# Optimization experiments

Measured on AMD Instinct MI355X. Metric: run time of the kernel, lower is better.

## Reference

```python
import jax, jax.numpy as jnp
import numpy as np

N, T = 1024, 32
D_FEAT, GATE_START, GATE_END = 158, 158, 221
D_MODEL = 256
T_NHEAD, S_NHEAD = 4, 2
BETA = 5.0
LN_EPS = 1e-5


def _ln(x, g, b):
    mu = jnp.mean(x, axis=-1, keepdims=True)
    var = jnp.mean(jnp.square(x - mu), axis=-1, keepdims=True)
    return (x - mu) * jax.lax.rsqrt(var + LN_EPS) * g + b


def _pos_enc(t, d):
    pos = jnp.arange(t, dtype=jnp.float32)[:, None]
    div = jnp.exp(jnp.arange(0, d, 2, dtype=jnp.float32) * (-np.log(10000.0) / d))
    pe = jnp.zeros((t, d), dtype=jnp.float32)
    pe = pe.at[:, 0::2].set(jnp.sin(pos * div))
    pe = pe.at[:, 1::2].set(jnp.cos(pos * div))
    return pe


def _mha(xn, qw, kw, vw, nhead, temperature):
    # xn: [B, S, D] (already layer-normed); attention over axis S
    B, S, D = xn.shape
    dh = D // nhead
    q = (xn @ qw.T).reshape(B, S, nhead, dh)
    k = (xn @ kw.T).reshape(B, S, nhead, dh)
    v = (xn @ vw.T).reshape(B, S, nhead, dh)
    scores = jnp.einsum('bshd,bthd->bhst', q, k) / temperature
    a = jax.nn.softmax(scores, axis=-1)
    return jnp.einsum('bhst,bthd->bshd', a, v).reshape(B, S, D)


def _block(x, qw, kw, vw, n1g, n1b, n2g, n2b, f1w, f1b, f2w, f2b, nhead, temperature):
    xn = _ln(x, n1g, n1b)
    xt = xn + _mha(xn, qw, kw, vw, nhead, temperature)
    xt = _ln(xt, n2g, n2b)
    ffn = jnp.maximum(xt @ f1w.T + f1b, 0.0) @ f2w.T + f2b
    return xt + ffn


def _forward(x, gate_w, gate_b, proj_w, proj_b,
             tq, tk, tv, tn1g, tn1b, tn2g, tn2b, tf1w, tf1b, tf2w, tf2b,
             sq, sk, sv, sn1g, sn1b, sn2g, sn2b, sf1w, sf1b, sf2w, sf2b,
             temp_w, out_w, out_b):
    src = x[:, :, :GATE_START]                     # [N, T, d_feat]
    gate_in = x[:, -1, GATE_START:GATE_END]        # [N, d_gate]
    gate = D_FEAT * jax.nn.softmax((gate_in @ gate_w.T + gate_b) / BETA, axis=-1)
    src = src * gate[:, None, :]
    z = src @ proj_w.T + proj_b                    # [N, T, d_model]
    z = z + _pos_enc(z.shape[1], D_MODEL)
    # TAttention: attend over time, unscaled scores (temperature=1)
    z = _block(z, tq, tk, tv, tn1g, tn1b, tn2g, tn2b, tf1w, tf1b, tf2w, tf2b,
               T_NHEAD, 1.0)
    # SAttention: attend over stocks, temperature = sqrt(d_model/nhead)
    zs = _block(z.swapaxes(0, 1), sq, sk, sv, sn1g, sn1b, sn2g, sn2b,
                sf1w, sf1b, sf2w, sf2b, S_NHEAD, float(np.sqrt(D_MODEL / S_NHEAD)))
    z = zs.swapaxes(0, 1)                          # [N, T, d_model]
    # TemporalAttention pooling
    h = z @ temp_w.T
    lam = jax.nn.softmax(jnp.einsum('ntd,nd->nt', h, h[:, -1, :]), axis=1)
    pooled = jnp.einsum('nt,ntd->nd', lam, z)
    return (pooled @ out_w.T + out_b).squeeze(-1)  # [N]


def setup_inputs() -> dict:
    key = jax.random.key(0)
    ks = iter(jax.random.split(key, 32))
    s = 0.02
    d, f, g = D_MODEL, D_FEAT, GATE_END - GATE_START
    inp = {
        'x': jax.random.normal(next(ks), (N, T, GATE_END), dtype=jnp.float32),
        'gate_w': jax.random.normal(next(ks), (f, g)) * s,
        'gate_b': jnp.zeros((f,)),
        'proj_w': jax.random.normal(next(ks), (d, f)) * s,
        'proj_b': jnp.zeros((d,)),
        'tq': jax.random.normal(next(ks), (d, d)) * s,
        'tk': jax.random.normal(next(ks), (d, d)) * s,
        'tv': jax.random.normal(next(ks), (d, d)) * s,
        'tn1g': jnp.ones((d,)), 'tn1b': jnp.zeros((d,)),
        'tn2g': jnp.ones((d,)), 'tn2b': jnp.zeros((d,)),
        'tf1w': jax.random.normal(next(ks), (d, d)) * s, 'tf1b': jnp.zeros((d,)),
        'tf2w': jax.random.normal(next(ks), (d, d)) * s, 'tf2b': jnp.zeros((d,)),
        'sq': jax.random.normal(next(ks), (d, d)) * s,
        'sk': jax.random.normal(next(ks), (d, d)) * s,
        'sv': jax.random.normal(next(ks), (d, d)) * s,
        'sn1g': jnp.ones((d,)), 'sn1b': jnp.zeros((d,)),
        'sn2g': jnp.ones((d,)), 'sn2b': jnp.zeros((d,)),
        'sf1w': jax.random.normal(next(ks), (d, d)) * s, 'sf1b': jnp.zeros((d,)),
        'sf2w': jax.random.normal(next(ks), (d, d)) * s, 'sf2b': jnp.zeros((d,)),
        'temp_w': jax.random.normal(next(ks), (d, d)) * s,
        'out_w': jax.random.normal(next(ks), (1, d)) * s,
        'out_b': jnp.zeros((1,)),
    }
    return {k: v.astype(jnp.float32) for k, v in inp.items()}


def reference(x, gate_w, gate_b, proj_w, proj_b,
              tq, tk, tv, tn1g, tn1b, tn2g, tn2b, tf1w, tf1b, tf2w, tf2b,
              sq, sk, sv, sn1g, sn1b, sn2g, sn2b, sf1w, sf1b, sf2w, sf2b,
              temp_w, out_w, out_b):
    return _forward(x, gate_w, gate_b, proj_w, proj_b,
                    tq, tk, tv, tn1g, tn1b, tn2g, tn2b, tf1w, tf1b, tf2w, tf2b,
                    sq, sk, sv, sn1g, sn1b, sn2g, sn2b, sf1w, sf1b, sf2w, sf2b,
                    temp_w, out_w, out_b)
```

## Files before the change

### kernel.cpp

```cpp
#include <hip/hip_runtime.h>
#include <math.h>

#define NB   1024
#define TSEQ 32
#define DM   256
#define DF   158
#define GDIM 63
#define XROW 221

typedef unsigned short u16;
typedef __attribute__((ext_vector_type(8))) __bf16 bf16x8;
typedef __attribute__((ext_vector_type(4))) float f32x4;
#define MFMA16(a,b,c) __builtin_amdgcn_mfma_f32_16x16x32_bf16(a,b,c,0,0,0)

#define MODE_QKVT 1
#define MODE_QKVS 2

__device__ __forceinline__ u16 f2bf(float f){
  union { float f; unsigned int u; } c; c.f = f;
  unsigned int u = c.u;
  u += 0x7fffu + ((u >> 16) & 1u);
  return (u16)(u >> 16);
}

__device__ __forceinline__ u16 f2bf_t(float f){
  union { float f; unsigned int u; } c; c.f = f;
  return (u16)(c.u >> 16);
}

__device__ __forceinline__ void gl2lds16(const u16* g, u16* lds_wave_base, int lane){
#if __has_builtin(__builtin_amdgcn_global_load_lds)
  __builtin_amdgcn_global_load_lds(
      (const __attribute__((address_space(1))) unsigned int*)g,
      (__attribute__((address_space(3))) unsigned int*)lds_wave_base,
      16, 0, 0);
#else
  *reinterpret_cast<uint4*>(lds_wave_base + lane * 8) =
      *reinterpret_cast<const uint4*>(g);
#endif
}

#define WB_TOT 770048

__global__ __launch_bounds__(256) void kConvAll(
    const float* __restrict__ tq, const float* __restrict__ tk, const float* __restrict__ tv,
    const float* __restrict__ sq, const float* __restrict__ sk, const float* __restrict__ sv,
    const float* __restrict__ tf1, const float* __restrict__ tf2,
    const float* __restrict__ sf1, const float* __restrict__ sf2,
    const float* __restrict__ tw, const float* __restrict__ pw,
    u16* __restrict__ WB)
{
  int i = blockIdx.x * 256 + threadIdx.x;
  if (i >= WB_TOT) return;
  if (i < 720896){
    int j = i >> 16, o = i & 65535;
    const float* s;
    switch (j){
      case 0: s = tq; break;  case 1: s = tk; break;  case 2: s = tv; break;
      case 3: s = sq; break;  case 4: s = sk; break;  case 5: s = sv; break;
      case 6: s = tf1; break; case 7: s = tf2; break;
      case 8: s = sf1; break; case 9: s = sf2; break;
      default: s = tw; break;
    }
    WB[i] = f2bf(s[o]);
  } else {
    int k = i - 720896;
    int row = k / 192, col = k - row * 192;
    WB[i] = (col < DF) ? f2bf(pw[row * DF + col]) : (u16)0;
  }
}


__global__ __launch_bounds__(256) void kGateSrc(
    const float* __restrict__ x,
    const float* __restrict__ gate_w, const float* __restrict__ gate_b,
    u16* __restrict__ SRC)
{
  __shared__ float s_gate[DF];
  __shared__ float s_gi[GDIM];
  const int tid = threadIdx.x;
  const int n = blockIdx.x;

  if (tid < GDIM) s_gi[tid] = x[(n * TSEQ + (TSEQ - 1)) * XROW + DF + tid];
  __syncthreads();
  float logit = 0.f;
  if (tid < DF){
    logit = gate_b[tid];
    const float* __restrict__ wr = gate_w + tid * GDIM;
    for (int g = 0; g < GDIM; ++g) logit += s_gi[g] * wr[g];
    logit *= 0.2f;
    s_gate[tid] = logit;
  }
  __syncthreads();
  {
    float mx = -1e30f;
    for (int f = 0; f < DF; ++f) mx = fmaxf(mx, s_gate[f]);
    float sm = 0.f;
    for (int f = 0; f < DF; ++f) sm += __expf(s_gate[f] - mx);
    __syncthreads();
    if (tid < DF) s_gate[tid] = (float)DF * __expf(logit - mx) / sm;
  }
  __syncthreads();

  for (int e = tid; e < TSEQ * 192; e += 256){
    int t = e / 192, f = e - t * 192;
    float v = 0.f;
    if (f < DF) v = x[(n * TSEQ + t) * XROW + f] * s_gate[f];
    SRC[(size_t)(n * TSEQ + t) * 192 + f] = f2bf(v);
  }
}


__global__ __launch_bounds__(512) void kProjLN(
    const u16* __restrict__ SRC, const u16* __restrict__ Bw,
    const float* __restrict__ bias,
    const float* __restrict__ lg, const float* __restrict__ lb,
    u16* __restrict__ Xb, float* __restrict__ Xf)
{
  __shared__ alignas(16) u16 sA[128 * 64];
  __shared__ alignas(16) u16 sB[256 * 64];
  __shared__ float s_sum[4 * 128], s_sq[4 * 128];
  __shared__ float s_lg[256], s_lb[256], s_bias[256];

  const int tid = threadIdx.x;
  const int wv = tid >> 6, lane = tid & 63;
  const int wr = wv >> 2, wc = wv & 3;
  const int quad = lane >> 4, lc = lane & 15;
  const int m0 = blockIdx.x * 128;

  if (tid < 256){ s_lg[tid] = lg[tid]; s_lb[tid] = lb[tid]; s_bias[tid] = bias[tid]; }

  f32x4 acc[4][4];
  #pragma unroll
  for (int i = 0; i < 4; ++i)
    #pragma unroll
    for (int j = 0; j < 4; ++j) acc[i][j] = (f32x4){0.f,0.f,0.f,0.f};

  for (int kt = 0; kt < 192; kt += 64){
    __syncthreads();
    #pragma unroll
    for (int i = 0; i < 2; ++i){
      int c = tid + i * 512;
      int row = c >> 3, blk = c & 7;
      *reinterpret_cast<uint4*>(&sA[row * 64 + ((blk ^ (row & 7)) * 8)]) =
        *reinterpret_cast<const uint4*>(SRC + (size_t)(m0 + row) * 192 + kt + blk * 8);
    }
    #pragma unroll
    for (int i = 0; i < 4; ++i){
      int c = tid + i * 512;
      int row = c >> 3, blk = c & 7;
      *reinterpret_cast<uint4*>(&sB[row * 64 + ((blk ^ (row & 7)) * 8)]) =
        *reinterpret_cast<const uint4*>(Bw + (size_t)row * 192 + kt + blk * 8);
    }
    __syncthreads();
    #pragma unroll
    for (int kc = 0; kc < 2; ++kc){
      const int sw = ((kc * 4 + quad) ^ (lc & 7)) * 8;
      bf16x8 a[4], b[4];
      #pragma unroll
      for (int i = 0; i < 4; ++i){
        a[i] = *reinterpret_cast<const bf16x8*>(&sA[(wr * 64 + i * 16 + lc) * 64 + sw]);
        b[i] = *reinterpret_cast<const bf16x8*>(&sB[(wc * 64 + i * 16 + lc) * 64 + sw]);
      }
      #pragma unroll
      for (int i = 0; i < 4; ++i)
        #pragma unroll
        for (int j = 0; j < 4; ++j)
          acc[i][j] = MFMA16(a[i], b[j], acc[i][j]);
    }
  }

  const int rb = wr * 64 + quad * 4;
  #pragma unroll
  for (int i = 0; i < 4; ++i)
    #pragma unroll
    for (int r = 0; r < 4; ++r){
      int rowl = rb + i * 16 + r;
      float ft = (float)((m0 + rowl) & 31);
      float ps = 0.f, pq = 0.f;
      #pragma unroll
      for (int j = 0; j < 4; ++j){
        int col = wc * 64 + j * 16 + lc;
        float div = __expf((float)(col & ~1) * -0.035977892f);
        float ang = ft * div;
        float pe = (col & 1) ? __cosf(ang) : __sinf(ang);
        float v = acc[i][j][r] + s_bias[col] + pe;
        acc[i][j][r] = v;
        ps += v; pq += v * v;
      }
      #pragma unroll
      for (int msk = 1; msk < 16; msk <<= 1){
        ps += __shfl_xor(ps, msk);
        pq += __shfl_xor(pq, msk);
      }
      if (lc == 0){ s_sum[wc * 128 + rowl] = ps; s_sq[wc * 128 + rowl] = pq; }
    }
  __syncthreads();

  #pragma unroll
  for (int i = 0; i < 4; ++i)
    #pragma unroll
    for (int r = 0; r < 4; ++r){
      int rowl = rb + i * 16 + r;
      float sum = s_sum[rowl] + s_sum[128 + rowl] + s_sum[256 + rowl] + s_sum[384 + rowl];
      float sq  = s_sq[rowl]  + s_sq[128 + rowl]  + s_sq[256 + rowl]  + s_sq[384 + rowl];
      float mu = sum * (1.f / 256.f);
      float rs = rsqrtf(sq * (1.f / 256.f) - mu * mu + 1e-5f);
      size_t base = (size_t)(m0 + rowl) * 256;
      #pragma unroll
      for (int j = 0; j < 4; ++j){
        int col = wc * 64 + j * 16 + lc;
        float xn = (acc[i][j][r] - mu) * rs * s_lg[col] + s_lb[col];
        Xf[base + col] = xn;
        Xb[base + col] = f2bf(xn);
      }
    }
}


__global__ __launch_bounds__(256) void gemm_bf16(
    const u16* __restrict__ A, const u16* __restrict__ B,
    const int K, const int mode,
    u16* __restrict__ ob0, u16* __restrict__ ob1, u16* __restrict__ ob2)
{
  __shared__ alignas(16) u16 sA[128 * 64];
  __shared__ alignas(16) u16 sB[128 * 64];
  const int tid = threadIdx.x;
  const int wv = tid >> 6, lane = tid & 63;
  const int wr = wv >> 1, wc = wv & 1;
  const int quad = lane >> 4, lc = lane & 15;
  const int n0 = blockIdx.y * 128;
  const bool tmaj = (mode == MODE_QKVS);
  const int tt = tmaj ? (blockIdx.x & 31) : 0;
  const int nb = tmaj ? (blockIdx.x >> 5) : 0;
  const int m0 = tmaj ? 0 : blockIdx.x * 128;

  f32x4 acc[4][4];
  #pragma unroll
  for (int i = 0; i < 4; ++i)
    #pragma unroll
    for (int j = 0; j < 4; ++j) acc[i][j] = (f32x4){0.f,0.f,0.f,0.f};

  for (int kt = 0; kt < K; kt += 64){
    __syncthreads();
    #pragma unroll
    for (int j = 0; j < 4; ++j){
      int c = wv * 64 + lane + j * 256;
      int row = c >> 3, blk = c & 7;
      int arow = tmaj ? ((nb * 128 + row) * 32 + tt) : (m0 + row);
      gl2lds16(A + (size_t)arow * K + kt + ((blk ^ (row & 7)) * 8),
               &sA[(wv * 64 + j * 256) * 8], lane);
      gl2lds16(B + (size_t)(n0 + row) * K + kt + ((blk ^ (row & 7)) * 8),
               &sB[(wv * 64 + j * 256) * 8], lane);
    }
    __syncthreads();
    #pragma unroll
    for (int kc = 0; kc < 2; ++kc){
      const int sw = ((kc * 4 + quad) ^ (lc & 7)) * 8;
      bf16x8 a[4], b[4];
      #pragma unroll
      for (int i = 0; i < 4; ++i){
        a[i] = *reinterpret_cast<const bf16x8*>(&sA[(wr * 64 + i * 16 + lc) * 64 + sw]);
        b[i] = *reinterpret_cast<const bf16x8*>(&sB[(wc * 64 + i * 16 + lc) * 64 + sw]);
      }
      #pragma unroll
      for (int i = 0; i < 4; ++i)
        #pragma unroll
        for (int j = 0; j < 4; ++j)
          acc[i][j] = MFMA16(a[i], b[j], acc[i][j]);
    }
  }

  const int rb = wr * 64 + quad * 4;
  const int cb = wc * 64 + lc;

  if (mode == MODE_QKVT){
    #pragma unroll
    for (int i = 0; i < 4; ++i)
      #pragma unroll
      for (int r = 0; r < 4; ++r){
        int row = m0 + rb + i * 16 + r;
        #pragma unroll
        for (int j = 0; j < 4; ++j){
          int col = n0 + cb + j * 16;
          int sel = col >> 8, c = col & 255;
          u16 v = f2bf(acc[i][j][r]);
          if (sel == 0)      ob0[(size_t)row * 256 + c] = v;
          else if (sel == 1) ob1[(size_t)row * 256 + c] = v;
          else {
            int h = c >> 6, dd = c & 63;
            ob2[(((size_t)(row >> 5) * 4 + h) * 64 + dd) * 32 + (row & 31)] = v;
          }
        }
      }
  } else {
    #pragma unroll
    for (int i = 0; i < 4; ++i)
      #pragma unroll
      for (int r = 0; r < 4; ++r){
        int rl = rb + i * 16 + r;
        int n = nb * 128 + rl;
        #pragma unroll
        for (int j = 0; j < 4; ++j){
          int col = n0 + cb + j * 16;
          int sel = col >> 8, c = col & 255;
          u16 v = f2bf(acc[i][j][r]);
          if (sel == 0)      ob0[((size_t)tt * NB + n) * 256 + c] = v;
          else if (sel == 1) ob1[((size_t)tt * NB + n) * 256 + c] = v;
          else {
            int h = c >> 7, dd = c & 127;
            ob2[(((size_t)tt * 2 + h) * 128 + dd) * NB + n] = v;
          }
        }
      }
  }
}


__global__ __launch_bounds__(512) void kFFN(
    const float* __restrict__ X,
    const float* __restrict__ lg, const float* __restrict__ lb,
    const u16* __restrict__ w1, const float* __restrict__ b1,
    const u16* __restrict__ w2, const float* __restrict__ b2,
    const float* __restrict__ og, const float* __restrict__ ob,
    float* __restrict__ outf, u16* __restrict__ obdual)
{
  __shared__ alignas(16) u16 sAB[24576];
  __shared__ alignas(16) u16 s_h1[128 * 256];
  __shared__ float s_mu[128], s_rs[128];
  __shared__ float s_lg[256], s_lb[256], s_b1[256], s_b2[256];
  __shared__ float s_og[256], s_ob[256];
  __shared__ float s_os[2 * 128], s_oq[2 * 128];

  const int tid = threadIdx.x;
  const int wv = tid >> 6, lane = tid & 63;
  const int quad = lane >> 4, lc = lane & 15;
  const int m0 = blockIdx.x * 128;
  const int m0w = (wv >> 1) * 32;
  const int n0w = (wv & 1) * 128;
  u16* sA = sAB;
  u16* sB = sAB + 8192;

  if (tid < 256){
    s_lg[tid] = lg[tid]; s_lb[tid] = lb[tid];
    s_b1[tid] = b1[tid]; s_b2[tid] = b2[tid];
    if (og){ s_og[tid] = og[tid]; s_ob[tid] = ob[tid]; }
  }

  {
    const int row = tid >> 2, j = tid & 3;
    const float4* xr = reinterpret_cast<const float4*>(X + (size_t)(m0 + row) * 256);
    float sum = 0.f, sq = 0.f;
    #pragma unroll
    for (int k = 0; k < 16; ++k){
      float4 v = xr[j + 4 * k];
      sum += v.x + v.y + v.z + v.w;
      sq  += v.x*v.x + v.y*v.y + v.z*v.z + v.w*v.w;
    }
    sum += __shfl_xor(sum, 1); sq += __shfl_xor(sq, 1);
    sum += __shfl_xor(sum, 2); sq += __shfl_xor(sq, 2);
    if (j == 0){
      float mu = sum * (1.f / 256.f);
      s_mu[row] = mu;
      s_rs[row] = rsqrtf(sq * (1.f / 256.f) - mu * mu + 1e-5f);
    }
  }
  __syncthreads();

  f32x4 acc[2][8];
  #pragma unroll
  for (int mt = 0; mt < 2; ++mt)
    #pragma unroll
    for (int j = 0; j < 8; ++j) acc[mt][j] = (f32x4){0.f,0.f,0.f,0.f};

  for (int kt = 0; kt < 4; ++kt){
    __syncthreads();
    {
      const int row = tid >> 2, c0 = (tid & 3) * 16;
      const float mu = s_mu[row], rs = s_rs[row];
      const float* xp = X + (size_t)(m0 + row) * 256 + kt * 64 + c0;
      u16 v16[16];
      #pragma unroll
      for (int k = 0; k < 4; ++k){
        float4 v = *reinterpret_cast<const float4*>(xp + 4 * k);
        int col = kt * 64 + c0 + 4 * k;
        v16[4*k+0] = f2bf((v.x - mu) * rs * s_lg[col+0] + s_lb[col+0]);
        v16[4*k+1] = f2bf((v.y - mu) * rs * s_lg[col+1] + s_lb[col+1]);
        v16[4*k+2] = f2bf((v.z - mu) * rs * s_lg[col+2] + s_lb[col+2]);
        v16[4*k+3] = f2bf((v.w - mu) * rs * s_lg[col+3] + s_lb[col+3]);
      }
      int b0 = c0 >> 3;
      *reinterpret_cast<uint4*>(&sA[row * 64 + ((b0    ) ^ (row & 7)) * 8]) = *reinterpret_cast<uint4*>(&v16[0]);
      *reinterpret_cast<uint4*>(&sA[row * 64 + ((b0 + 1) ^ (row & 7)) * 8]) = *reinterpret_cast<uint4*>(&v16[8]);
    }
    #pragma unroll
    for (int i = 0; i < 4; ++i){
      int c = tid + i * 512;
      int row = c >> 3, blk = c & 7;
      *reinterpret_cast<uint4*>(&sB[row * 64 + (blk ^ (row & 7)) * 8]) =
        *reinterpret_cast<const uint4*>(w1 + (size_t)row * 256 + kt * 64 + blk * 8);
    }
    __syncthreads();
    #pragma unroll
    for (int kc = 0; kc < 2; ++kc){
      const int sw = ((kc * 4 + quad) ^ (lc & 7)) * 8;
      bf16x8 a[2], b[8];
      #pragma unroll
      for (int mt = 0; mt < 2; ++mt)
        a[mt] = *reinterpret_cast<const bf16x8*>(&sA[(m0w + mt * 16 + lc) * 64 + sw]);
      #pragma unroll
      for (int j = 0; j < 8; ++j)
        b[j] = *reinterpret_cast<const bf16x8*>(&sB[(n0w + j * 16 + lc) * 64 + sw]);
      #pragma unroll
      for (int mt = 0; mt < 2; ++mt)
        #pragma unroll
        for (int j = 0; j < 8; ++j)
          acc[mt][j] = MFMA16(a[mt], b[j], acc[mt][j]);
    }
  }
  __syncthreads();

  #pragma unroll
  for (int mt = 0; mt < 2; ++mt)
    #pragma unroll
    for (int r = 0; r < 4; ++r){
      int row = m0w + mt * 16 + quad * 4 + r;
      #pragma unroll
      for (int j = 0; j < 8; ++j){
        int col = n0w + j * 16 + lc;
        u16 v = f2bf(fmaxf(acc[mt][j][r] + s_b1[col], 0.f));
        s_h1[row * 256 + (((col >> 3) ^ (row & 31)) << 3) + (col & 7)] = v;
      }
    }

  #pragma unroll
  for (int mt = 0; mt < 2; ++mt)
    #pragma unroll
    for (int j = 0; j < 8; ++j) acc[mt][j] = (f32x4){0.f,0.f,0.f,0.f};

  for (int kt = 0; kt < 4; ++kt){
    __syncthreads();
    #pragma unroll
    for (int i = 0; i < 4; ++i){
      int c = tid + i * 512;
      int row = c >> 3, blk = c & 7;
      *reinterpret_cast<uint4*>(&sAB[row * 64 + (blk ^ (row & 7)) * 8]) =
        *reinterpret_cast<const uint4*>(w2 + (size_t)row * 256 + kt * 64 + blk * 8);
    }
    __syncthreads();
    #pragma unroll
    for (int kc = 0; kc < 2; ++kc){
      const int sw = ((kc * 4 + quad) ^ (lc & 7)) * 8;
      bf16x8 a[2], b[8];
      #pragma unroll
      for (int mt = 0; mt < 2; ++mt){
        int row = m0w + mt * 16 + lc;
        int cb = kt * 8 + kc * 4 + quad;
        a[mt] = *reinterpret_cast<const bf16x8*>(
            &s_h1[row * 256 + ((cb ^ (row & 31)) << 3)]);
      }
      #pragma unroll
      for (int j = 0; j < 8; ++j)
        b[j] = *reinterpret_cast<const bf16x8*>(&sAB[(n0w + j * 16 + lc) * 64 + sw]);
      #pragma unroll
      for (int mt = 0; mt < 2; ++mt)
        #pragma unroll
        for (int j = 0; j < 8; ++j)
          acc[mt][j] = MFMA16(a[mt], b[j], acc[mt][j]);
    }
  }

  if (og){
    #pragma unroll
    for (int mt = 0; mt < 2; ++mt)
      #pragma unroll
      for (int r = 0; r < 4; ++r){
        int rowl = m0w + mt * 16 + quad * 4 + r;
        const float mu = s_mu[rowl], rs = s_rs[rowl];
        size_t base = (size_t)(m0 + rowl) * 256;
        float ps = 0.f, pq = 0.f;
        #pragma unroll
        for (int j = 0; j < 8; ++j){
          int col = n0w + j * 16 + lc;
          float xn = (X[base + col] - mu) * rs * s_lg[col] + s_lb[col];
          float v = acc[mt][j][r] + s_b2[col] + xn;
          acc[mt][j][r] = v;
          ps += v; pq += v * v;
        }
        #pragma unroll
        for (int msk = 1; msk < 16; msk <<= 1){
          ps += __shfl_xor(ps, msk);
          pq += __shfl_xor(pq, msk);
        }
        if (lc == 0){
          s_os[(wv & 1) * 128 + rowl] = ps;
          s_oq[(wv & 1) * 128 + rowl] = pq;
        }
      }
    __syncthreads();
    #pragma unroll
    for (int mt = 0; mt < 2; ++mt)
      #pragma unroll
      for (int r = 0; r < 4; ++r){
        int rowl = m0w + mt * 16 + quad * 4 + r;
        float sum = s_os[rowl] + s_os[128 + rowl];
        float sq  = s_oq[rowl] + s_oq[128 + rowl];
        float mu2 = sum * (1.f / 256.f);
        float rs2 = rsqrtf(sq * (1.f / 256.f) - mu2 * mu2 + 1e-5f);
        size_t base = (size_t)(m0 + rowl) * 256;
        #pragma unroll
        for (int j = 0; j < 8; ++j){
          int col = n0w + j * 16 + lc;
          float w = (acc[mt][j][r] - mu2) * rs2 * s_og[col] + s_ob[col];
          outf[base + col] = w;
          obdual[base + col] = f2bf(w);
        }
      }
  } else {
    #pragma unroll
    for (int mt = 0; mt < 2; ++mt)
      #pragma unroll
      for (int r = 0; r < 4; ++r){
        int rowl = m0w + mt * 16 + quad * 4 + r;
        const float mu = s_mu[rowl], rs = s_rs[rowl];
        size_t base = (size_t)(m0 + rowl) * 256;
        #pragma unroll
        for (int j = 0; j < 8; ++j){
          int col = n0w + j * 16 + lc;
          float xn = (X[base + col] - mu) * rs * s_lg[col] + s_lb[col];
          float v = acc[mt][j][r] + s_b2[col] + xn;
          outf[base + col] = v;
          if (obdual) obdual[base + col] = f2bf(v);
        }
      }
  }
}


__global__ __launch_bounds__(256) void kAttnT(
    const u16* __restrict__ Qt, const u16* __restrict__ Kt,
    const u16* __restrict__ VtT, const float* __restrict__ XN1f,
    float* __restrict__ X2)
{
  __shared__ alignas(16) u16 sQ[4][32 * 72];
  __shared__ alignas(16) u16 sK[4][32 * 72];
  __shared__ alignas(16) u16 sV[4][64 * 40];
  __shared__ alignas(16) u16 sP[4][32 * 40];

  const int tid = threadIdx.x;
  const int wv = tid >> 6, lane = tid & 63;
  const int quad = lane >> 4, lc = lane & 15;
  const int n = blockIdx.x;
  const int h = wv;
  const f32x4 zero4 = {0.f, 0.f, 0.f, 0.f};

  #pragma unroll
  for (int i = 0; i < 4; ++i){
    int c = lane + 64 * i;
    int row = c >> 3, blk = c & 7;
    *reinterpret_cast<uint4*>(&sQ[wv][row * 72 + blk * 8]) =
      *reinterpret_cast<const uint4*>(&Qt[((size_t)n * 32 + row) * 256 + h * 64 + blk * 8]);
    *reinterpret_cast<uint4*>(&sK[wv][row * 72 + blk * 8]) =
      *reinterpret_cast<const uint4*>(&Kt[((size_t)n * 32 + row) * 256 + h * 64 + blk * 8]);
    int rv = c >> 2, bv = c & 3;
    *reinterpret_cast<uint4*>(&sV[wv][rv * 40 + bv * 8]) =
      *reinterpret_cast<const uint4*>(&VtT[(((size_t)n * 4 + h) * 64 + rv) * 32 + bv * 8]);
  }
  __syncthreads();

  f32x4 s[2][2];
  #pragma unroll
  for (int mt = 0; mt < 2; ++mt)
    #pragma unroll
    for (int ct = 0; ct < 2; ++ct) s[mt][ct] = zero4;
  #pragma unroll
  for (int kc = 0; kc < 2; ++kc){
    bf16x8 aq[2], bk[2];
    #pragma unroll
    for (int mt = 0; mt < 2; ++mt)
      aq[mt] = *reinterpret_cast<const bf16x8*>(&sQ[wv][(mt * 16 + lc) * 72 + kc * 32 + quad * 8]);
    #pragma unroll
    for (int ct = 0; ct < 2; ++ct)
      bk[ct] = *reinterpret_cast<const bf16x8*>(&sK[wv][(ct * 16 + lc) * 72 + kc * 32 + quad * 8]);
    #pragma unroll
    for (int mt = 0; mt < 2; ++mt)
      #pragma unroll
      for (int ct = 0; ct < 2; ++ct)
        s[mt][ct] = MFMA16(aq[mt], bk[ct], s[mt][ct]);
  }

  #pragma unroll
  for (int mt = 0; mt < 2; ++mt){
    #pragma unroll
    for (int r = 0; r < 4; ++r){
      float v0 = s[mt][0][r], v1 = s[mt][1][r];
      float mx = fmaxf(v0, v1);
      #pragma unroll
      for (int msk = 1; msk < 16; msk <<= 1) mx = fmaxf(mx, __shfl_xor(mx, msk));
      float p0 = __expf(v0 - mx), p1 = __expf(v1 - mx);
      float sm = p0 + p1;
      #pragma unroll
      for (int msk = 1; msk < 16; msk <<= 1) sm += __shfl_xor(sm, msk);
      float inv = 1.f / sm;
      sP[wv][(mt * 16 + quad * 4 + r) * 40 + lc]      = f2bf(p0 * inv);
      sP[wv][(mt * 16 + quad * 4 + r) * 40 + lc + 16] = f2bf(p1 * inv);
    }
  }
  __syncthreads();

  #pragma unroll
  for (int mt = 0; mt < 2; ++mt){
    bf16x8 ap = *reinterpret_cast<const bf16x8*>(&sP[wv][(mt * 16 + lc) * 40 + quad * 8]);
    #pragma unroll
    for (int ct = 0; ct < 4; ++ct){
      bf16x8 bv = *reinterpret_cast<const bf16x8*>(&sV[wv][(ct * 16 + lc) * 40 + quad * 8]);
      f32x4 o = MFMA16(ap, bv, zero4);
      #pragma unroll
      for (int r = 0; r < 4; ++r){
        int t = mt * 16 + quad * 4 + r;
        size_t idx = ((size_t)n * 32 + t) * 256 + h * 64 + ct * 16 + lc;
        X2[idx] = XN1f[idx] + o[r];
      }
    }
  }
}


__global__ __launch_bounds__(512) void kB2_flash_mfma(
    const u16* __restrict__ Qh, const u16* __restrict__ Kh,
    const u16* __restrict__ VT, const float* __restrict__ XNs,
    float* __restrict__ XT)
{
  __shared__ alignas(16) u16 smem[46080];

  const int tid = threadIdx.x;
  const int wv = tid >> 6, lane = tid & 63;
  const int wq = wv & 3, wk = wv >> 2;
  const int quad = lane >> 4, lc = lane & 15;
  const int t = blockIdx.x >> 1, h = blockIdx.x & 1;
  const int n0 = blockIdx.y * 128;
  const float c_exp2 = 0.12752887f;
  const int qb = n0 + wq * 32;

  bf16x8 qf[2][4];
  #pragma unroll
  for (int mt = 0; mt < 2; ++mt){
    const u16* qp = Qh + ((size_t)(t * NB + qb + mt * 16 + lc)) * DM + h * 128 + quad * 8;
    #pragma unroll
    for (int kc = 0; kc < 4; ++kc)
      qf[mt][kc] = *reinterpret_cast<const bf16x8*>(qp + kc * 32);
  }

  f32x4 o[2][8];
  #pragma unroll
  for (int mt = 0; mt < 2; ++mt)
    #pragma unroll
    for (int f = 0; f < 8; ++f) o[mt][f] = (f32x4){0.f, 0.f, 0.f, 0.f};
  float l_acc[2][4] = {{0.f,0.f,0.f,0.f},{0.f,0.f,0.f,0.f}};

  const u16* kbase  = Kh + (size_t)t * NB * DM + h * 128;
  const u16* vtbase = VT + (size_t)(t * 2 + h) * 128 * NB;
  u16* pw = smem + 35840 + wv * 1280;

  const int krow0 = tid >> 4,          kpart = tid & 15;
  const int vrow0 = tid >> 3,          vpart = tid & 7;

  uint4 rk[2], rv[2];
  #pragma unroll
  for (int it = 0; it < 2; ++it){
    rk[it] = *reinterpret_cast<const uint4*>(kbase + (size_t)(krow0 + it * 32) * DM + kpart * 8);
    rv[it] = *reinterpret_cast<const uint4*>(vtbase + (size_t)(vrow0 + it * 64) * NB + 0 + vpart * 8);
  }
  #pragma unroll
  for (int it = 0; it < 2; ++it){
    *reinterpret_cast<uint4*>(&smem[(size_t)0 + (krow0 + it * 32) * 136 + kpart * 8]) = rk[it];
    *reinterpret_cast<uint4*>(&smem[17408 + (vrow0 + it * 64) * 72 + vpart * 8]) = rv[it];
  }

  for (int jt = 0; jt < 16; ++jt){
    const int j1 = (jt + 1) * 64;
    if (jt + 1 < 16){
      #pragma unroll
      for (int it = 0; it < 2; ++it){
        rk[it] = *reinterpret_cast<const uint4*>(kbase + (size_t)(j1 + krow0 + it * 32) * DM + kpart * 8);
        rv[it] = *reinterpret_cast<const uint4*>(vtbase + (size_t)(vrow0 + it * 64) * NB + j1 + vpart * 8);
      }
    }
    __syncthreads();
    const int b = jt & 1;
    u16* s_k  = smem + b * 8704;
    u16* s_vt = smem + 17408 + b * 9216;

    f32x4 s[2][2];
    #pragma unroll
    for (int mt = 0; mt < 2; ++mt)
      #pragma unroll
      for (int nt = 0; nt < 2; ++nt) s[mt][nt] = (f32x4){0.f,0.f,0.f,0.f};
    #pragma unroll
    for (int kc = 0; kc < 4; ++kc){
      #pragma unroll
      for (int nt = 0; nt < 2; ++nt){
        bf16x8 bk = *reinterpret_cast<const bf16x8*>(
            &s_k[(lc + 16 * nt + 32 * wk) * 136 + kc * 32 + quad * 8]);
        #pragma unroll
        for (int mt = 0; mt < 2; ++mt)
          s[mt][nt] = MFMA16(qf[mt][kc], bk, s[mt][nt]);
      }
    }

    #pragma unroll
    for (int mt = 0; mt < 2; ++mt)
      #pragma unroll
      for (int nt = 0; nt < 2; ++nt)
        #pragma unroll
        for (int r = 0; r < 4; ++r){
          float p = exp2f(s[mt][nt][r] * c_exp2);
          l_acc[mt][r] += p;
          pw[(mt * 16 + quad * 4 + r) * 40 + lc + 16 * nt] = f2bf_t(p);
        }

    bf16x8 ap[2];
    #pragma unroll
    for (int mt = 0; mt < 2; ++mt)
      ap[mt] = *reinterpret_cast<const bf16x8*>(&pw[(mt * 16 + lc) * 40 + quad * 8]);
    #pragma unroll
    for (int f = 0; f < 8; ++f){
      bf16x8 bv = *reinterpret_cast<const bf16x8*>(
          &s_vt[(lc + 16 * f) * 72 + 32 * wk + quad * 8]);
      #pragma unroll
      for (int mt = 0; mt < 2; ++mt)
        o[mt][f] = MFMA16(ap[mt], bv, o[mt][f]);
    }

    if (jt + 1 < 16){
      const int nb2 = (jt + 1) & 1;
      u16* d_k  = smem + nb2 * 8704;
      u16* d_vt = smem + 17408 + nb2 * 9216;
      #pragma unroll
      for (int it = 0; it < 2; ++it){
        *reinterpret_cast<uint4*>(&d_k[(krow0 + it * 32) * 136 + kpart * 8]) = rk[it];
        *reinterpret_cast<uint4*>(&d_vt[(vrow0 + it * 64) * 72 + vpart * 8]) = rv[it];
      }
    }
  }

  float* fo = (float*)smem;
  float* fl = (float*)smem + 8192;

  __syncthreads();
  if (wk == 1){
    int base = (wq * 64 + lane) * 32;
    #pragma unroll
    for (int f = 0; f < 8; ++f)
      #pragma unroll
      for (int r = 0; r < 4; ++r) fo[base + f * 4 + r] = o[0][f][r];
    int lb = (wq * 64 + lane) * 8;
    #pragma unroll
    for (int mt = 0; mt < 2; ++mt)
      #pragma unroll
      for (int r = 0; r < 4; ++r) fl[lb + mt * 4 + r] = l_acc[mt][r];
  }
  __syncthreads();
  if (wk == 0){
    int base = (wq * 64 + lane) * 32;
    #pragma unroll
    for (int f = 0; f < 8; ++f)
      #pragma unroll
      for (int r = 0; r < 4; ++r) o[0][f][r] += fo[base + f * 4 + r];
    int lb = (wq * 64 + lane) * 8;
    #pragma unroll
    for (int mt = 0; mt < 2; ++mt)
      #pragma unroll
      for (int r = 0; r < 4; ++r){
        l_acc[mt][r] += fl[lb + mt * 4 + r];
        #pragma unroll
        for (int msk = 1; msk < 16; msk <<= 1)
          l_acc[mt][r] += __shfl_xor(l_acc[mt][r], msk);
      }
    #pragma unroll
    for (int r = 0; r < 4; ++r){
      float linv = 1.f / l_acc[0][r];
      int row = qb + quad * 4 + r;
      size_t xnb = ((size_t)row * TSEQ + t) * DM + h * 128 + lc;
      size_t xtb = ((size_t)t * NB + row) * DM + h * 128 + lc;
      #pragma unroll
      for (int f = 0; f < 8; ++f)
        XT[xtb + f * 16] = XNs[xnb + f * 16] + o[0][f][r] * linv;
    }
  }
  __syncthreads();
  if (wk == 1){
    int base = (wq * 64 + lane) * 32;
    #pragma unroll
    for (int f = 0; f < 8; ++f)
      #pragma unroll
      for (int r = 0; r < 4; ++r) fo[base + f * 4 + r] = o[1][f][r];
  }
  __syncthreads();
  if (wk == 0){
    int base = (wq * 64 + lane) * 32;
    #pragma unroll
    for (int f = 0; f < 8; ++f)
      #pragma unroll
      for (int r = 0; r < 4; ++r) o[1][f][r] += fo[base + f * 4 + r];
    #pragma unroll
    for (int r = 0; r < 4; ++r){
      float linv = 1.f / l_acc[1][r];
      int row = qb + 16 + quad * 4 + r;
      size_t xnb = ((size_t)row * TSEQ + t) * DM + h * 128 + lc;
      size_t xtb = ((size_t)t * NB + row) * DM + h * 128 + lc;
      #pragma unroll
      for (int f = 0; f < 8; ++f)
        XT[xtb + f * 16] = XNs[xnb + f * 16] + o[1][f][r] * linv;
    }
  }
}


__global__ __launch_bounds__(256) void kC_pool(
    const u16* __restrict__ ZSb, const float* __restrict__ ZSf,
    const u16* __restrict__ Wt,
    const float* __restrict__ out_w, const float* __restrict__ out_b,
    float* __restrict__ out)
{
  __shared__ alignas(16) unsigned char smem[66448];
  float* s_h  = (float*)smem;
  u16*   s_zb = (u16*)(smem + 33280);
  float* s_z  = (float*)(smem + 33280);
  float* s_sc = (float*)(smem + 33280 + 32768);
  float* s_red = s_sc + 32;

  const int tid = threadIdx.x;
  const int wv = tid >> 6, lane = tid & 63;
  const int quad = lane >> 4, lc = lane & 15;
  const int n = blockIdx.x;

  {
    const int row = tid >> 3, part = tid & 7;
    const u16* src = ZSb + ((size_t)row * NB + n) * 256 + part * 32;
    #pragma unroll
    for (int k = 0; k < 4; ++k)
      *reinterpret_cast<uint4*>(&s_zb[row * 264 + part * 32 + k * 8]) =
        *reinterpret_cast<const uint4*>(src + k * 8);
  }
  __syncthreads();

  {
    f32x4 acc[2][4];
    #pragma unroll
    for (int mt = 0; mt < 2; ++mt)
      #pragma unroll
      for (int ct = 0; ct < 4; ++ct) acc[mt][ct] = (f32x4){0.f,0.f,0.f,0.f};
    #pragma unroll
    for (int kc = 0; kc < 8; ++kc){
      bf16x8 a[2];
      #pragma unroll
      for (int mt = 0; mt < 2; ++mt)
        a[mt] = *reinterpret_cast<const bf16x8*>(&s_zb[(mt * 16 + lc) * 264 + kc * 32 + quad * 8]);
      #pragma unroll
      for (int ct = 0; ct < 4; ++ct){
        bf16x8 b = *reinterpret_cast<const bf16x8*>(
            Wt + (size_t)(wv * 64 + ct * 16 + lc) * 256 + kc * 32 + quad * 8);
        #pragma unroll
        for (int mt = 0; mt < 2; ++mt)
          acc[mt][ct] = MFMA16(a[mt], b, acc[mt][ct]);
      }
    }
    __syncthreads();
    #pragma unroll
    for (int mt = 0; mt < 2; ++mt)
      #pragma unroll
      for (int ct = 0; ct < 4; ++ct)
        #pragma unroll
        for (int r = 0; r < 4; ++r)
          s_h[(mt * 16 + quad * 4 + r) * 260 + wv * 64 + ct * 16 + lc] = acc[mt][ct][r];
  }

  for (int e = tid; e < 32 * DM; e += 256){
    int i = e >> 8, dd = e & 255;
    s_z[i * 256 + dd] = ZSf[((size_t)i * NB + n) * DM + dd];
  }
  __syncthreads();

  {
    const int s = tid >> 3, j = tid & 7;
    float acc = 0.f;
    #pragma unroll
    for (int k = 0; k < DM; k += 8) acc += s_h[s * 260 + k + j] * s_h[31 * 260 + k + j];
    #pragma unroll
    for (int o = 1; o < 8; o <<= 1) acc += __shfl_xor(acc, o);
    if (j == 0) s_sc[s] = acc;
  }
  __syncthreads();

  float mx = -1e30f;
  #pragma unroll
  for (int s = 0; s < 32; ++s) mx = fmaxf(mx, s_sc[s]);
  float sm = 0.f;
  #pragma unroll
  for (int s = 0; s < 32; ++s) sm += __expf(s_sc[s] - mx);
  const float inv = 1.f / sm;

  const int d = tid;
  float pooled = 0.f;
  #pragma unroll
  for (int s = 0; s < 32; ++s) pooled += __expf(s_sc[s] - mx) * inv * s_z[s * 256 + d];

  float val = pooled * out_w[d];
  #pragma unroll
  for (int o = 1; o < 64; o <<= 1) val += __shfl_xor(val, o);
  if ((tid & 63) == 0) s_red[tid >> 6] = val;
  __syncthreads();
  if (tid == 0) out[n] = s_red[0] + s_red[1] + s_red[2] + s_red[3] + out_b[0];
}


extern "C" void kernel_launch(void* const* d_in, const int* in_sizes, int n_in,
                              void* d_out, int out_size, void* d_ws, size_t ws_size,
                              hipStream_t stream)
{
  const float* x      = (const float*)d_in[0];
  const float* gate_w = (const float*)d_in[1];
  const float* gate_b = (const float*)d_in[2];
  const float* proj_w = (const float*)d_in[3];
  const float* proj_b = (const float*)d_in[4];
  const float* tq   = (const float*)d_in[5];
  const float* tk   = (const float*)d_in[6];
  const float* tv   = (const float*)d_in[7];
  const float* tn1g = (const float*)d_in[8];
  const float* tn1b = (const float*)d_in[9];
  const float* tn2g = (const float*)d_in[10];
  const float* tn2b = (const float*)d_in[11];
  const float* tf1w = (const float*)d_in[12];
  const float* tf1b = (const float*)d_in[13];
  const float* tf2w = (const float*)d_in[14];
  const float* tf2b = (const float*)d_in[15];
  const float* sq   = (const float*)d_in[16];
  const float* sk   = (const float*)d_in[17];
  const float* sv   = (const float*)d_in[18];
  const float* sn1g = (const float*)d_in[19];
  const float* sn1b = (const float*)d_in[20];
  const float* sn2g = (const float*)d_in[21];
  const float* sn2b = (const float*)d_in[22];
  const float* sf1w = (const float*)d_in[23];
  const float* sf1b = (const float*)d_in[24];
  const float* sf2w = (const float*)d_in[25];
  const float* sf2b = (const float*)d_in[26];
  const float* temp_w = (const float*)d_in[27];
  const float* out_w  = (const float*)d_in[28];
  const float* out_b  = (const float*)d_in[29];

  float* W = (float*)d_ws;
  const size_t F = (size_t)NB * TSEQ * DM;

  float* Z  = W;
  float* XF = W + F;
  u16* U0 = (u16*)(W + 2 * F);
  u16* U1 = (u16*)(W + 2 * F) + F;
  u16* U2 = (u16*)(W + 3 * F);
  u16* U3 = (u16*)(W + 3 * F) + F;
  u16* SRC = (u16*)(W + 4 * F);
  u16* WB  = (u16*)(W + 4 * F + 3145728 + 4096);

  kConvAll<<<(WB_TOT + 255) / 256, 256, 0, stream>>>(
      tq, tk, tv, sq, sk, sv, tf1w, tf2w, sf1w, sf2w, temp_w, proj_w, WB);
  kGateSrc<<<NB, 256, 0, stream>>>(x, gate_w, gate_b, SRC);
  kProjLN<<<256, 512, 0, stream>>>(SRC, WB + 720896, proj_b, tn1g, tn1b, U0, XF);
  gemm_bf16<<<dim3(256, 6), 256, 0, stream>>>(U0, WB, 256, MODE_QKVT, U1, U2, U3);
  kAttnT<<<NB, 256, 0, stream>>>(U1, U2, U3, XF, Z);
  kFFN<<<256, 512, 0, stream>>>(Z, tn2g, tn2b, WB + 393216, tf1b,
      WB + 458752, tf2b, sn1g, sn1b, XF, U2);
  gemm_bf16<<<dim3(256, 6), 256, 0, stream>>>(U2, WB + 196608, 256, MODE_QKVS, U3, U1, U0);
  kB2_flash_mfma<<<dim3(64, 8), 512, 0, stream>>>(U3, U1, U0, XF, Z);
  kFFN<<<256, 512, 0, stream>>>(Z, sn2g, sn2b, WB + 524288, sf1b,
      WB + 589824, sf2b, nullptr, nullptr, Z, U0);
  kC_pool<<<NB, 256, 0, stream>>>(U0, Z, WB + 655360, out_w, out_b, (float*)d_out);
}
```

Before: 478.4 us.

## Replace double-buffered K/V prefetch with single-buffered synchronous loads in flash kernel

The spatial-attention flash kernel drops its register-prefetched double-buffered K and V^T tiles in favour of a single shared buffer that is loaded directly at the top of each 64-key iteration between two barriers. This shrinks LDS use from about 90KB to about 56KB per block, which could let more blocks reside per CU and frees the prefetch registers. In exchange, global load latency is no longer hidden behind the MFMA work of the previous tile, and each iteration now has an extra barrier.

```diff
diff --git a/kernel.cpp b/kernel.cpp
--- a/kernel.cpp
+++ b/kernel.cpp
@@ -631,7 +631,10 @@
     const u16* __restrict__ VT, const float* __restrict__ XNs,
     float* __restrict__ XT)
 {
-  __shared__ alignas(16) u16 smem[46080];
+  __shared__ alignas(16) u16 smem[28160];
+  u16* s_k  = smem;
+  u16* s_vt = smem + 8704;
+  u16* s_p  = smem + 17920;
 
   const int tid = threadIdx.x;
   const int wv = tid >> 6, lane = tid & 63;
@@ -660,36 +663,21 @@
 
   const u16* kbase  = Kh + (size_t)t * NB * DM + h * 128;
   const u16* vtbase = VT + (size_t)(t * 2 + h) * 128 * NB;
-  u16* pw = smem + 35840 + wv * 1280;
-
-  const int krow0 = tid >> 4,          kpart = tid & 15;
-  const int vrow0 = tid >> 3,          vpart = tid & 7;
-
-  uint4 rk[2], rv[2];
-  #pragma unroll
-  for (int it = 0; it < 2; ++it){
-    rk[it] = *reinterpret_cast<const uint4*>(kbase + (size_t)(krow0 + it * 32) * DM + kpart * 8);
-    rv[it] = *reinterpret_cast<const uint4*>(vtbase + (size_t)(vrow0 + it * 64) * NB + 0 + vpart * 8);
-  }
-  #pragma unroll
-  for (int it = 0; it < 2; ++it){
-    *reinterpret_cast<uint4*>(&smem[(size_t)0 + (krow0 + it * 32) * 136 + kpart * 8]) = rk[it];
-    *reinterpret_cast<uint4*>(&smem[17408 + (vrow0 + it * 64) * 72 + vpart * 8]) = rv[it];
-  }
-
-  for (int jt = 0; jt < 16; ++jt){
-    const int j1 = (jt + 1) * 64;
-    if (jt + 1 < 16){
-      #pragma unroll
-      for (int it = 0; it < 2; ++it){
-        rk[it] = *reinterpret_cast<const uint4*>(kbase + (size_t)(j1 + krow0 + it * 32) * DM + kpart * 8);
-        rv[it] = *reinterpret_cast<const uint4*>(vtbase + (size_t)(vrow0 + it * 64) * NB + j1 + vpart * 8);
-      }
-    }
-    __syncthreads();
-    const int b = jt & 1;
-    u16* s_k  = smem + b * 8704;
-    u16* s_vt = smem + 17408 + b * 9216;
+  u16* pw = s_p + wv * 1280;
+
+  for (int j0 = 0; j0 < NB; j0 += 64){
+    __syncthreads();
+    #pragma unroll
+    for (int it = 0; it < 2; ++it){
+      int c = tid + it * 512;
+      int row = c >> 4, part = c & 15;
+      *reinterpret_cast<uint4*>(&s_k[row * 136 + part * 8]) =
+        *reinterpret_cast<const uint4*>(kbase + (size_t)(j0 + row) * DM + part * 8);
+      int rv = c >> 3, pv = c & 7;
+      *reinterpret_cast<uint4*>(&s_vt[rv * 72 + pv * 8]) =
+        *reinterpret_cast<const uint4*>(vtbase + (size_t)rv * NB + j0 + pv * 8);
+    }
+    __syncthreads();
 
     f32x4 s[2][2];
     #pragma unroll
@@ -730,17 +718,6 @@
       #pragma unroll
       for (int mt = 0; mt < 2; ++mt)
         o[mt][f] = MFMA16(ap[mt], bv, o[mt][f]);
-    }
-
-    if (jt + 1 < 16){
-      const int nb2 = (jt + 1) & 1;
-      u16* d_k  = smem + nb2 * 8704;
-      u16* d_vt = smem + 17408 + nb2 * 9216;
-      #pragma unroll
-      for (int it = 0; it < 2; ++it){
-        *reinterpret_cast<uint4*>(&d_k[(krow0 + it * 32) * 136 + kpart * 8]) = rk[it];
-        *reinterpret_cast<uint4*>(&d_vt[(vrow0 + it * 64) * 72 + vpart * 8]) = rv[it];
-      }
     }
   }
 
```

New measurement: 450.8 us. 1.06x faster.
